# Kernel tuning notes

Hardware: AMD Instinct MI355X
Metric: run time of the kernel (lower is better)

Reference implementation:

```python
import jax, jax.numpy as jnp
import numpy as np

N_HEADS = 8
D_MODEL = 256
HEAD_DEPTH = D_MODEL // N_HEADS
B, S = 2, 4096


def setup_inputs() -> dict:
    key = jax.random.key(0)
    ks = jax.random.split(key, 8)
    scale = 1.0 / np.sqrt(D_MODEL)
    return {
        "q": jax.random.normal(ks[0], (B, S, D_MODEL), dtype=jnp.float32),
        "k": jax.random.normal(ks[1], (B, S, D_MODEL), dtype=jnp.float32),
        "v": jax.random.normal(ks[2], (B, S, D_MODEL), dtype=jnp.float32),
        "mask": jax.random.randint(ks[3], (B, S, S), 0, 2).astype(jnp.bool_),
        "wq": jax.random.normal(ks[4], (D_MODEL, D_MODEL), dtype=jnp.float32) * scale,
        "wk": jax.random.normal(ks[5], (D_MODEL, D_MODEL), dtype=jnp.float32) * scale,
        "wv": jax.random.normal(ks[6], (D_MODEL, D_MODEL), dtype=jnp.float32) * scale,
        "w_out": jax.random.normal(ks[7], (D_MODEL, D_MODEL), dtype=jnp.float32) * scale,
    }


def _split_heads(x):
    # [B, S, D] -> [B, H, S, Dh]
    b, s, _ = x.shape
    return x.reshape(b, s, N_HEADS, HEAD_DEPTH).transpose(0, 2, 1, 3)


def reference(q, k, v, mask, wq, wk, wv, w_out):
    Q = _split_heads(q @ wq)
    K = _split_heads(k @ wk)
    V = _split_heads(v @ wv)
    # [B, H, Sq, Sk]
    scores = jnp.einsum('bhqd,bhkd->bhqk', Q, K) / jnp.sqrt(
        jnp.asarray(HEAD_DEPTH, dtype=Q.dtype))
    # mask True -> -inf, broadcast over heads
    scores = jnp.where(mask[:, None, :, :], -jnp.inf, scores)
    probs = jax.nn.softmax(scores, axis=-1)
    attn = jnp.einsum('bhqk,bhkd->bhqd', probs, V)
    attn = attn.transpose(0, 2, 1, 3).reshape(q.shape[0], -1, D_MODEL)
    return attn @ w_out
```

## Files before the change

kernel.cpp:

```cpp
#include <hip/hip_runtime.h>
#include <stdint.h>

typedef __bf16 bf16;
typedef __bf16 bf16x8 __attribute__((ext_vector_type(8)));
typedef __bf16 bf16x4 __attribute__((ext_vector_type(4)));
typedef float  f32x4  __attribute__((ext_vector_type(4)));
typedef float  float4v __attribute__((ext_vector_type(4)));
typedef unsigned int uint;
typedef unsigned long long ull;

#define QSCALE 0.25505003984214403f

__global__ __launch_bounds__(256) void transpose_w(
    const float* __restrict__ w0, const float* __restrict__ w1,
    const float* __restrict__ w2, const float* __restrict__ w3,
    bf16* __restrict__ WT) {
  const int wsel = blockIdx.z;
  const float* W = wsel == 0 ? w0 : wsel == 1 ? w1 : wsel == 2 ? w2 : w3;
  const int k0 = blockIdx.x * 64, n0 = blockIdx.y * 64;
  __shared__ __align__(16) bf16 t[64][72];
  const int tid = threadIdx.x;
  {
    const int kk = (tid >> 4) << 2;
    const int nn = (tid & 15) << 2;
#pragma unroll
    for (int r = 0; r < 4; ++r) {
      float4v a = *(const float4v*)(W + (size_t)(k0 + kk + r) * 256 + n0 + nn);
#pragma unroll
      for (int j = 0; j < 4; ++j) t[nn + j][kk + r] = (bf16)a[j];
    }
  }
  __syncthreads();
  {
    const int ni = tid >> 2;
    const int c  = (tid & 3) * 16;
    bf16x8 o0 = *(const bf16x8*)(&t[ni][c]);
    bf16x8 o1 = *(const bf16x8*)(&t[ni][c + 8]);
    bf16* dst = WT + (size_t)wsel * 65536 + (size_t)(n0 + ni) * 256 + k0 + c;
    *(bf16x8*)dst = o0;
    *(bf16x8*)(dst + 8) = o1;
  }
}

__global__ __launch_bounds__(256) void pack_mask(const int* __restrict__ mask,
                                                 ull* __restrict__ out) {
  const int wid = blockIdx.x * 4 + (threadIdx.x >> 6);
  const int lane = threadIdx.x & 63;
  const size_t base = (size_t)wid * 1024 + lane;
  ull b[16];
#pragma unroll
  for (int j = 0; j < 16; ++j) b[j] = __ballot(mask[base + 64 * j] != 0);
  if (lane == 0) {
    ulonglong2* o = (ulonglong2*)(out + (size_t)wid * 16);
#pragma unroll
    for (int j = 0; j < 8; ++j) { ulonglong2 v; v.x = b[2 * j]; v.y = b[2 * j + 1]; o[j] = v; }
  }
}

__global__ __launch_bounds__(256) void proj_kernel(
    const float* __restrict__ xq, const float* __restrict__ xk, const float* __restrict__ xv,
    const bf16* __restrict__ WT,
    bf16* __restrict__ Qo, bf16* __restrict__ Ko, bf16* __restrict__ Vt) {
  const int z = blockIdx.z;
  const float* X = z == 0 ? xq : (z == 1 ? xk : xv);
  const bf16* wt = WT + (size_t)z * 65536;
  const int m0 = blockIdx.x * 64, n0 = blockIdx.y * 128;
  const int tid = threadIdx.x, wave = tid >> 6, lane = tid & 63;
  const int nl = lane & 15, quad = lane >> 4;
  const int arow = m0 + wave * 16 + nl;
  const float* xrow = X + (size_t)arow * 256;

  f32x4 zero4 = {0.f, 0.f, 0.f, 0.f};
  f32x4 acc[8];
#pragma unroll
  for (int i = 0; i < 8; ++i) acc[i] = zero4;

  for (int ks = 0; ks < 8; ++ks) {
    float4v a0 = *(const float4v*)(xrow + ks * 32 + quad * 8);
    float4v a1 = *(const float4v*)(xrow + ks * 32 + quad * 8 + 4);
    bf16x8 af;
#pragma unroll
    for (int i = 0; i < 4; ++i) { af[i] = (bf16)a0[i]; af[4 + i] = (bf16)a1[i]; }
#pragma unroll
    for (int nf = 0; nf < 8; ++nf) {
      bf16x8 bfr = *(const bf16x8*)(wt + (size_t)(n0 + nf * 16 + nl) * 256 + ks * 32 + quad * 8);
      acc[nf] = __builtin_amdgcn_mfma_f32_16x16x32_bf16(af, bfr, acc[nf], 0, 0, 0);
    }
  }

  const int Rbase = m0 + wave * 16 + quad * 4;
  if (z == 2) {
    const int b = Rbase >> 12, s = Rbase & 4095;
#pragma unroll
    for (int nf = 0; nf < 8; ++nf) {
      const int col = n0 + nf * 16 + nl;
      const int h = col >> 5, d = col & 31;
      bf16x4 o;
#pragma unroll
      for (int r = 0; r < 4; ++r) o[r] = (bf16)acc[nf][r];
      *(bf16x4*)(Vt + (((size_t)(b * 8 + h)) * 32 + d) * 4096 + s) = o;
    }
  } else {
    const float scale = (z == 0) ? QSCALE : 1.0f;
    bf16* Out = z == 0 ? Qo : Ko;
#pragma unroll
    for (int nf = 0; nf < 8; ++nf) {
      const int col = n0 + nf * 16 + nl;
      const int h = col >> 5, d = col & 31;
#pragma unroll
      for (int r = 0; r < 4; ++r) {
        const int R = Rbase + r;
        const int b = R >> 12, s = R & 4095;
        Out[(((size_t)(b * 8 + h)) * 4096 + s) * 32 + d] = (bf16)(acc[nf][r] * scale);
      }
    }
  }
}

__global__ __launch_bounds__(256, 6) void attn_kernel(
    const bf16* __restrict__ Qg, const bf16* __restrict__ Kg,
    const bf16* __restrict__ Vtg, const uint* __restrict__ Mg,
    bf16* __restrict__ Og) {
  const int bh = blockIdx.y, b = bh >> 3, h = bh & 7;
  const int q0 = blockIdx.x * 64;
  const int tid = threadIdx.x, wave = tid >> 6, lane = tid & 63;
  const int nl = lane & 15, quad = lane >> 4, q4 = quad * 4;

  __shared__ __align__(16) bf16 Klds[128 * 32];
  __shared__ __align__(16) bf16 Vlds[32 * 136];
  __shared__ __align__(16) bf16 Plds[4][16 * 72];

  const int qrow = q0 + wave * 16 + nl;
  const bf16x8 qf = *(const bf16x8*)(Qg + ((size_t)bh * 4096 + qrow) * 32 + quad * 8);
  const uint* mrow = Mg + ((size_t)b * 4096 + qrow) * 128;
  const bf16* Kbase = Kg + (size_t)bh * 4096 * 32;
  const bf16* Vbase = Vtg + (size_t)bh * 32 * 4096;

  f32x4 zero4 = {0.f, 0.f, 0.f, 0.f};
  f32x4 acc0 = zero4, acc1 = zero4, accl = zero4;
  bf16x8 ones;
#pragma unroll
  for (int i = 0; i < 8; ++i) ones[i] = (bf16)1.0f;

  bf16* pw = &Plds[wave][nl * 72 + q4];
  const bf16* pr = &Plds[wave][nl * 72 + quad * 8];
  const int vd = tid >> 4, vk = (tid & 15) * 8;

  for (int kt = 0; kt < 32; ++kt) {
    const bf16* kc = Kbase + kt * 4096;
    *(bf16x8*)(Klds + tid * 8)        = *(const bf16x8*)(kc + tid * 8);
    *(bf16x8*)(Klds + 2048 + tid * 8) = *(const bf16x8*)(kc + 2048 + tid * 8);
    const bf16* vc = Vbase + kt * 128 + vk;
    *(bf16x8*)(Vlds + vd * 136 + vk)        = *(const bf16x8*)(vc + (size_t)vd * 4096);
    *(bf16x8*)(Vlds + (vd + 16) * 136 + vk) = *(const bf16x8*)(vc + (size_t)(vd + 16) * 4096);
    __syncthreads();

    const uint4 mq = *(const uint4*)(mrow + kt * 4);

#pragma unroll
    for (int h2 = 0; h2 < 2; ++h2) {
      const uint ks0 = (~(h2 ? mq.z : mq.x)) >> q4;
      const uint ks1 = (~(h2 ? mq.w : mq.y)) >> q4;

      f32x4 st[4];
#pragma unroll
      for (int t = 0; t < 4; ++t) {
        bf16x8 a = *(const bf16x8*)(Klds + ((h2 * 4 + t) * 16 + nl) * 32 + quad * 8);
        st[t] = __builtin_amdgcn_mfma_f32_16x16x32_bf16(a, qf, zero4, 0, 0, 0);
      }

#pragma unroll
      for (int t = 0; t < 4; ++t) {
        const uint ks = (t < 2) ? ks0 : ks1;
        const int off = (t & 1) * 16;
        bf16x4 p4;
#pragma unroll
        for (int r = 0; r < 4; ++r) {
          float e = __builtin_amdgcn_exp2f(st[t][r]);
          uint keep = (uint)__builtin_amdgcn_sbfe((int)ks, off + r, 1);
          e = __uint_as_float(__float_as_uint(e) & keep);
          p4[r] = (bf16)e;
        }
        *(bf16x4*)(pw + 16 * t) = p4;
      }

#pragma unroll
      for (int c = 0; c < 2; ++c) {
        bf16x8 pb  = *(const bf16x8*)(pr + c * 32);
        bf16x8 va0 = *(const bf16x8*)(Vlds + nl * 136 + h2 * 64 + c * 32 + quad * 8);
        bf16x8 va1 = *(const bf16x8*)(Vlds + (nl + 16) * 136 + h2 * 64 + c * 32 + quad * 8);
        acc0 = __builtin_amdgcn_mfma_f32_16x16x32_bf16(va0, pb, acc0, 0, 0, 0);
        acc1 = __builtin_amdgcn_mfma_f32_16x16x32_bf16(va1, pb, acc1, 0, 0, 0);
        accl = __builtin_amdgcn_mfma_f32_16x16x32_bf16(ones, pb, accl, 0, 0, 0);
      }
    }
    __syncthreads();
  }

  const float rl = 1.0f / accl[0];

  bf16x4 o0, o1;
#pragma unroll
  for (int r = 0; r < 4; ++r) { o0[r] = (bf16)(acc0[r] * rl); o1[r] = (bf16)(acc1[r] * rl); }
  bf16* obase = Og + ((size_t)(b * 4096 + qrow)) * 256 + h * 32 + q4;
  *(bf16x4*)obase = o0;
  *(bf16x4*)(obase + 16) = o1;
}

__global__ __launch_bounds__(256) void gemm_out(
    const bf16* __restrict__ A, const bf16* __restrict__ WTo, float* __restrict__ C) {
  const int m0 = blockIdx.x * 64, n0 = blockIdx.y * 128;
  const int tid = threadIdx.x, wave = tid >> 6, lane = tid & 63;
  const int nl = lane & 15, quad = lane >> 4;
  const int arow = m0 + wave * 16 + nl;

  f32x4 zero4 = {0.f, 0.f, 0.f, 0.f};
  f32x4 acc[8];
#pragma unroll
  for (int i = 0; i < 8; ++i) acc[i] = zero4;

  for (int ks = 0; ks < 8; ++ks) {
    bf16x8 af = *(const bf16x8*)(A + (size_t)arow * 256 + ks * 32 + quad * 8);
#pragma unroll
    for (int nf = 0; nf < 8; ++nf) {
      bf16x8 bfr = *(const bf16x8*)(WTo + (size_t)(n0 + nf * 16 + nl) * 256 + ks * 32 + quad * 8);
      acc[nf] = __builtin_amdgcn_mfma_f32_16x16x32_bf16(af, bfr, acc[nf], 0, 0, 0);
    }
  }
  const int Rbase = m0 + wave * 16 + quad * 4;
#pragma unroll
  for (int nf = 0; nf < 8; ++nf)
#pragma unroll
    for (int r = 0; r < 4; ++r)
      C[(size_t)(Rbase + r) * 256 + n0 + nf * 16 + nl] = acc[nf][r];
}

extern "C" void kernel_launch(void* const* d_in, const int* in_sizes, int n_in,
                              void* d_out, int out_size, void* d_ws, size_t ws_size,
                              hipStream_t stream) {
  const float* q  = (const float*)d_in[0];
  const float* k  = (const float*)d_in[1];
  const float* v  = (const float*)d_in[2];
  const int*  mask = (const int*)d_in[3];
  const float* wq = (const float*)d_in[4];
  const float* wk = (const float*)d_in[5];
  const float* wv = (const float*)d_in[6];
  const float* wo = (const float*)d_in[7];
  float* out = (float*)d_out;

  uint8_t* ws = (uint8_t*)d_ws;
  bf16* WT = (bf16*)ws;
  bf16* Qb = (bf16*)(ws + (512u << 10));
  bf16* Kb = Qb + 2097152;
  bf16* Vt = Kb + 2097152;
  ull*  Mb = (ull*)((uint8_t*)(Vt + 2097152));
  bf16* Ao = (bf16*)((uint8_t*)Mb + (4u << 20));

  transpose_w<<<dim3(4, 4, 4), 256, 0, stream>>>(wq, wk, wv, wo, WT);
  pack_mask<<<dim3(8192), 256, 0, stream>>>(mask, Mb);
  proj_kernel<<<dim3(128, 2, 3), 256, 0, stream>>>(q, k, v, WT, Qb, Kb, Vt);
  attn_kernel<<<dim3(64, 16), 256, 0, stream>>>(Qb, Kb, Vt, (const uint*)Mb, Ao);
  gemm_out<<<dim3(128, 2), 256, 0, stream>>>(Ao, WT + 3 * 65536, out);
}
```

Baseline: 349.3 us.

## Rewrite attention with 32x32 MFMA, key-split waves, and fuse mask packing into projection

The attention kernel drops LDS staging of K/V and per-tile barriers. Each wave now owns a 32-key slice of every tile and computes 64 queries with 32x32x16 MFMAs. Partial outputs and row sums are reduced across waves in shared memory at the end. The mask is packed in a transposed key-major layout and the packing is folded into the projection launch as extra blocks, which removes one kernel launch. The trade-off is larger register accumulators, direct global loads of K/V and mask, and a final cross-wave reduction.

Result: no change. 354.6 us (+1.5%).

```diff
diff --git a/kernel.cpp b/kernel.cpp
--- a/kernel.cpp
+++ b/kernel.cpp
@@ -5,6 +5,7 @@
 typedef __bf16 bf16x8 __attribute__((ext_vector_type(8)));
 typedef __bf16 bf16x4 __attribute__((ext_vector_type(4)));
 typedef float  f32x4  __attribute__((ext_vector_type(4)));
+typedef float  f32x16 __attribute__((ext_vector_type(16)));
 typedef float  float4v __attribute__((ext_vector_type(4)));
 typedef unsigned int uint;
 typedef unsigned long long ull;
@@ -42,30 +43,39 @@
   }
 }
 
-__global__ __launch_bounds__(256) void pack_mask(const int* __restrict__ mask,
-                                                 ull* __restrict__ out) {
-  const int wid = blockIdx.x * 4 + (threadIdx.x >> 6);
-  const int lane = threadIdx.x & 63;
-  const size_t base = (size_t)wid * 1024 + lane;
-  ull b[16];
-#pragma unroll
-  for (int j = 0; j < 16; ++j) b[j] = __ballot(mask[base + 64 * j] != 0);
-  if (lane == 0) {
-    ulonglong2* o = (ulonglong2*)(out + (size_t)wid * 16);
-#pragma unroll
-    for (int j = 0; j < 8; ++j) { ulonglong2 v; v.x = b[2 * j]; v.y = b[2 * j + 1]; o[j] = v; }
-  }
-}
-
-__global__ __launch_bounds__(256) void proj_kernel(
+__global__ __launch_bounds__(256) void proj_pack(
     const float* __restrict__ xq, const float* __restrict__ xk, const float* __restrict__ xv,
     const bf16* __restrict__ WT,
-    bf16* __restrict__ Qo, bf16* __restrict__ Ko, bf16* __restrict__ Vt) {
-  const int z = blockIdx.z;
+    bf16* __restrict__ Qo, bf16* __restrict__ Ko, bf16* __restrict__ Vt,
+    const int* __restrict__ mask, uint* __restrict__ M2) {
+  const int tid = threadIdx.x;
+  if (blockIdx.x >= 768) {
+    const int pid = blockIdx.x - 768;
+    const int wid = pid * 4 + (tid >> 6);
+    const int lane = tid & 63;
+    const int row = wid >> 2, chunk = wid & 3;
+    const int b = row >> 12, q = row & 4095;
+    const size_t base = (size_t)row * 4096 + chunk * 1024 + lane;
+    ull bl[16];
+#pragma unroll
+    for (int j = 0; j < 16; ++j) bl[j] = __ballot(mask[base + 64 * j] != 0);
+    if (lane == 0) {
+      uint* o = M2 + (size_t)b * 524288 + q;
+#pragma unroll
+      for (int j = 0; j < 16; ++j) {
+        const int kdw = chunk * 32 + 2 * j;
+        o[(size_t)kdw * 4096] = (uint)bl[j];
+        o[(size_t)(kdw + 1) * 4096] = (uint)(bl[j] >> 32);
+      }
+    }
+    return;
+  }
+  const int z = blockIdx.x >> 8;
+  const int r8 = blockIdx.x & 255;
+  const int m0 = (r8 >> 1) * 64, n0 = (r8 & 1) * 128;
   const float* X = z == 0 ? xq : (z == 1 ? xk : xv);
   const bf16* wt = WT + (size_t)z * 65536;
-  const int m0 = blockIdx.x * 64, n0 = blockIdx.y * 128;
-  const int tid = threadIdx.x, wave = tid >> 6, lane = tid & 63;
+  const int wave = tid >> 6, lane = tid & 63;
   const int nl = lane & 15, quad = lane >> 4;
   const int arow = m0 + wave * 16 + nl;
   const float* xrow = X + (size_t)arow * 256;
@@ -97,7 +107,7 @@
       const int h = col >> 5, d = col & 31;
       bf16x4 o;
 #pragma unroll
-      for (int r = 0; r < 4; ++r) o[r] = (bf16)acc[nf][r];
+      for (int rr = 0; rr < 4; ++rr) o[rr] = (bf16)acc[nf][rr];
       *(bf16x4*)(Vt + (((size_t)(b * 8 + h)) * 32 + d) * 4096 + s) = o;
     }
   } else {
@@ -108,103 +118,129 @@
       const int col = n0 + nf * 16 + nl;
       const int h = col >> 5, d = col & 31;
 #pragma unroll
-      for (int r = 0; r < 4; ++r) {
-        const int R = Rbase + r;
+      for (int rr = 0; rr < 4; ++rr) {
+        const int R = Rbase + rr;
         const int b = R >> 12, s = R & 4095;
-        Out[(((size_t)(b * 8 + h)) * 4096 + s) * 32 + d] = (bf16)(acc[nf][r] * scale);
+        Out[(((size_t)(b * 8 + h)) * 4096 + s) * 32 + d] = (bf16)(acc[nf][rr] * scale);
       }
     }
   }
 }
 
-__global__ __launch_bounds__(256, 6) void attn_kernel(
+__global__ __launch_bounds__(256) void attn_kernel(
     const bf16* __restrict__ Qg, const bf16* __restrict__ Kg,
-    const bf16* __restrict__ Vtg, const uint* __restrict__ Mg,
+    const bf16* __restrict__ Vtg, const uint* __restrict__ M2,
     bf16* __restrict__ Og) {
   const int bh = blockIdx.y, b = bh >> 3, h = bh & 7;
   const int q0 = blockIdx.x * 64;
-  const int tid = threadIdx.x, wave = tid >> 6, lane = tid & 63;
-  const int nl = lane & 15, quad = lane >> 4, q4 = quad * 4;
-
-  __shared__ __align__(16) bf16 Klds[128 * 32];
-  __shared__ __align__(16) bf16 Vlds[32 * 136];
-  __shared__ __align__(16) bf16 Plds[4][16 * 72];
-
-  const int qrow = q0 + wave * 16 + nl;
-  const bf16x8 qf = *(const bf16x8*)(Qg + ((size_t)bh * 4096 + qrow) * 32 + quad * 8);
-  const uint* mrow = Mg + ((size_t)b * 4096 + qrow) * 128;
-  const bf16* Kbase = Kg + (size_t)bh * 4096 * 32;
-  const bf16* Vbase = Vtg + (size_t)bh * 32 * 4096;
-
-  f32x4 zero4 = {0.f, 0.f, 0.f, 0.f};
-  f32x4 acc0 = zero4, acc1 = zero4, accl = zero4;
-  bf16x8 ones;
-#pragma unroll
-  for (int i = 0; i < 8; ++i) ones[i] = (bf16)1.0f;
-
-  bf16* pw = &Plds[wave][nl * 72 + q4];
-  const bf16* pr = &Plds[wave][nl * 72 + quad * 8];
-  const int vd = tid >> 4, vk = (tid & 15) * 8;
+  const int tid = threadIdx.x, w = tid >> 6, lane = tid & 63;
+  const int nl = lane & 31, half = lane >> 5;
+
+  __shared__ float Ored[4][32][66];
+  __shared__ float Lsum[64][8];
+
+  bf16x8 qf[2][2];
+  {
+    const bf16* Qbase = Qg + ((size_t)bh * 4096 + q0) * 32;
+#pragma unroll
+    for (int qt = 0; qt < 2; ++qt)
+#pragma unroll
+      for (int s = 0; s < 2; ++s)
+        qf[qt][s] = *(const bf16x8*)(Qbase + (size_t)(qt * 32 + nl) * 32 + s * 16 + half * 8);
+  }
+
+  const bf16* Kbase = Kg + (size_t)bh * 4096 * 32 + (size_t)(w * 32 + nl) * 32;
+  const bf16* Vbase = Vtg + ((size_t)bh * 32 + nl) * 4096 + w * 32 + half * 4;
+  const uint* Mbase = M2 + (size_t)b * 524288 + q0 + nl;
+
+  f32x16 acc0, acc1;
+#pragma unroll
+  for (int i = 0; i < 16; ++i) { acc0[i] = 0.f; acc1[i] = 0.f; }
+  float lsum0 = 0.f, lsum1 = 0.f;
 
   for (int kt = 0; kt < 32; ++kt) {
-    const bf16* kc = Kbase + kt * 4096;
-    *(bf16x8*)(Klds + tid * 8)        = *(const bf16x8*)(kc + tid * 8);
-    *(bf16x8*)(Klds + 2048 + tid * 8) = *(const bf16x8*)(kc + 2048 + tid * 8);
-    const bf16* vc = Vbase + kt * 128 + vk;
-    *(bf16x8*)(Vlds + vd * 136 + vk)        = *(const bf16x8*)(vc + (size_t)vd * 4096);
-    *(bf16x8*)(Vlds + (vd + 16) * 136 + vk) = *(const bf16x8*)(vc + (size_t)(vd + 16) * 4096);
-    __syncthreads();
-
-    const uint4 mq = *(const uint4*)(mrow + kt * 4);
-
-#pragma unroll
-    for (int h2 = 0; h2 < 2; ++h2) {
-      const uint ks0 = (~(h2 ? mq.z : mq.x)) >> q4;
-      const uint ks1 = (~(h2 ? mq.w : mq.y)) >> q4;
-
-      f32x4 st[4];
-#pragma unroll
-      for (int t = 0; t < 4; ++t) {
-        bf16x8 a = *(const bf16x8*)(Klds + ((h2 * 4 + t) * 16 + nl) * 32 + quad * 8);
-        st[t] = __builtin_amdgcn_mfma_f32_16x16x32_bf16(a, qf, zero4, 0, 0, 0);
+    const bf16* kc = Kbase + (size_t)kt * 4096;
+    bf16x8 ka0 = *(const bf16x8*)(kc + half * 8);
+    bf16x8 ka1 = *(const bf16x8*)(kc + 16 + half * 8);
+    const bf16* vc = Vbase + (size_t)kt * 128;
+    bf16x4 v00 = *(const bf16x4*)(vc);
+    bf16x4 v01 = *(const bf16x4*)(vc + 8);
+    bf16x4 v10 = *(const bf16x4*)(vc + 16);
+    bf16x4 v11 = *(const bf16x4*)(vc + 24);
+    bf16x8 va0, va1;
+#pragma unroll
+    for (int j = 0; j < 4; ++j) {
+      va0[j] = v00[j]; va0[4 + j] = v01[j];
+      va1[j] = v10[j]; va1[4 + j] = v11[j];
+    }
+    const uint* mp = Mbase + (size_t)(kt * 4 + w) * 4096;
+    const int minv0 = (int)((~mp[0]) >> (4 * half));
+    const int minv1 = (int)((~mp[32]) >> (4 * half));
+
+    f32x16 z16;
+#pragma unroll
+    for (int i = 0; i < 16; ++i) z16[i] = 0.f;
+    f32x16 st0 = __builtin_amdgcn_mfma_f32_32x32x16_bf16(ka0, qf[0][0], z16, 0, 0, 0);
+    st0 = __builtin_amdgcn_mfma_f32_32x32x16_bf16(ka1, qf[0][1], st0, 0, 0, 0);
+    f32x16 st1 = __builtin_amdgcn_mfma_f32_32x32x16_bf16(ka0, qf[1][0], z16, 0, 0, 0);
+    st1 = __builtin_amdgcn_mfma_f32_32x32x16_bf16(ka1, qf[1][1], st1, 0, 0, 0);
+
+    bf16 pe0[16], pe1[16];
+#pragma unroll
+    for (int g = 0; g < 4; ++g)
+#pragma unroll
+      for (int r = 0; r < 4; ++r) {
+        const int i = g * 4 + r, off = r + 8 * g;
+        float e0 = __builtin_amdgcn_exp2f(st0[i]);
+        float e1 = __builtin_amdgcn_exp2f(st1[i]);
+        const uint k0m = (uint)__builtin_amdgcn_sbfe(minv0, off, 1);
+        const uint k1m = (uint)__builtin_amdgcn_sbfe(minv1, off, 1);
+        e0 = __uint_as_float(__float_as_uint(e0) & k0m);
+        e1 = __uint_as_float(__float_as_uint(e1) & k1m);
+        lsum0 += e0; lsum1 += e1;
+        pe0[i] = (bf16)e0; pe1[i] = (bf16)e1;
       }
-
-#pragma unroll
-      for (int t = 0; t < 4; ++t) {
-        const uint ks = (t < 2) ? ks0 : ks1;
-        const int off = (t & 1) * 16;
-        bf16x4 p4;
-#pragma unroll
-        for (int r = 0; r < 4; ++r) {
-          float e = __builtin_amdgcn_exp2f(st[t][r]);
-          uint keep = (uint)__builtin_amdgcn_sbfe((int)ks, off + r, 1);
-          e = __uint_as_float(__float_as_uint(e) & keep);
-          p4[r] = (bf16)e;
-        }
-        *(bf16x4*)(pw + 16 * t) = p4;
-      }
-
-#pragma unroll
-      for (int c = 0; c < 2; ++c) {
-        bf16x8 pb  = *(const bf16x8*)(pr + c * 32);
-        bf16x8 va0 = *(const bf16x8*)(Vlds + nl * 136 + h2 * 64 + c * 32 + quad * 8);
-        bf16x8 va1 = *(const bf16x8*)(Vlds + (nl + 16) * 136 + h2 * 64 + c * 32 + quad * 8);
-        acc0 = __builtin_amdgcn_mfma_f32_16x16x32_bf16(va0, pb, acc0, 0, 0, 0);
-        acc1 = __builtin_amdgcn_mfma_f32_16x16x32_bf16(va1, pb, acc1, 0, 0, 0);
-        accl = __builtin_amdgcn_mfma_f32_16x16x32_bf16(ones, pb, accl, 0, 0, 0);
-      }
-    }
-    __syncthreads();
-  }
-
-  const float rl = 1.0f / accl[0];
-
-  bf16x4 o0, o1;
-#pragma unroll
-  for (int r = 0; r < 4; ++r) { o0[r] = (bf16)(acc0[r] * rl); o1[r] = (bf16)(acc1[r] * rl); }
-  bf16* obase = Og + ((size_t)(b * 4096 + qrow)) * 256 + h * 32 + q4;
-  *(bf16x4*)obase = o0;
-  *(bf16x4*)(obase + 16) = o1;
+    const bf16x8 pb00 = *(const bf16x8*)&pe0[0];
+    const bf16x8 pb01 = *(const bf16x8*)&pe0[8];
+    const bf16x8 pb10 = *(const bf16x8*)&pe1[0];
+    const bf16x8 pb11 = *(const bf16x8*)&pe1[8];
+
+    acc0 = __builtin_amdgcn_mfma_f32_32x32x16_bf16(va0, pb00, acc0, 0, 0, 0);
+    acc0 = __builtin_amdgcn_mfma_f32_32x32x16_bf16(va1, pb01, acc0, 0, 0, 0);
+    acc1 = __builtin_amdgcn_mfma_f32_32x32x16_bf16(va0, pb10, acc1, 0, 0, 0);
+    acc1 = __builtin_amdgcn_mfma_f32_32x32x16_bf16(va1, pb11, acc1, 0, 0, 0);
+  }
+
+#pragma unroll
+  for (int g = 0; g < 4; ++g)
+#pragma unroll
+    for (int r = 0; r < 4; ++r) {
+      const int d = r + 8 * g + 4 * half, i = g * 4 + r;
+      Ored[w][d][nl] = acc0[i];
+      Ored[w][d][32 + nl] = acc1[i];
+    }
+  Lsum[nl][w * 2 + half] = lsum0;
+  Lsum[32 + nl][w * 2 + half] = lsum1;
+  __syncthreads();
+  if (tid < 64) {
+    float s = 0.f;
+#pragma unroll
+    for (int j = 0; j < 8; ++j) s += Lsum[tid][j];
+    Lsum[tid][0] = 1.0f / s;
+  }
+  __syncthreads();
+  {
+    const int q = tid >> 2, db = (tid & 3) * 8;
+    const float rl = Lsum[q][0];
+    bf16x8 o;
+#pragma unroll
+    for (int dj = 0; dj < 8; ++dj) {
+      const float s = Ored[0][db + dj][q] + Ored[1][db + dj][q] +
+                      Ored[2][db + dj][q] + Ored[3][db + dj][q];
+      o[dj] = (bf16)(s * rl);
+    }
+    *(bf16x8*)(Og + ((size_t)(b * 4096 + q0 + q)) * 256 + h * 32 + db) = o;
+  }
 }
 
 __global__ __launch_bounds__(256) void gemm_out(
@@ -253,12 +289,11 @@
   bf16* Qb = (bf16*)(ws + (512u << 10));
   bf16* Kb = Qb + 2097152;
   bf16* Vt = Kb + 2097152;
-  ull*  Mb = (ull*)((uint8_t*)(Vt + 2097152));
+  uint* Mb = (uint*)((uint8_t*)(Vt + 2097152));
   bf16* Ao = (bf16*)((uint8_t*)Mb + (4u << 20));
 
   transpose_w<<<dim3(4, 4, 4), 256, 0, stream>>>(wq, wk, wv, wo, WT);
-  pack_mask<<<dim3(8192), 256, 0, stream>>>(mask, Mb);
-  proj_kernel<<<dim3(128, 2, 3), 256, 0, stream>>>(q, k, v, WT, Qb, Kb, Vt);
-  attn_kernel<<<dim3(64, 16), 256, 0, stream>>>(Qb, Kb, Vt, (const uint*)Mb, Ao);
+  proj_pack<<<dim3(768 + 8192), 256, 0, stream>>>(q, k, v, WT, Qb, Kb, Vt, mask, Mb);
+  attn_kernel<<<dim3(64, 16), 256, 0, stream>>>(Qb, Kb, Vt, Mb, Ao);
   gemm_out<<<dim3(128, 2), 256, 0, stream>>>(Ao, WT + 3 * 65536, out);
 }
```
